# Performance work log

Measured on AMD Instinct MI355X. Metric: run time of the kernel, lower is better.

Reference implementation:

```python
import jax, jax.numpy as jnp
import numpy as np

BN_EPS = 1e-5
GRID_W = 17  # conv output width hardcoded via lat_idx*17+lon_idx

def _conv(x, w, b, stride):
    y = jax.lax.conv_general_dilated(x, w, (stride, stride), [(1, 1), (1, 1)],
                                     dimension_numbers=("NCHW", "OIHW", "NCHW"))
    return y + b[None, :, None, None]

def _bn_eval(x, g, b):
    # running_mean=0, running_var=1 (fresh BatchNorm in eval mode)
    inv = jnp.float32(1.0 / np.sqrt(1.0 + BN_EPS))
    return x * (g[None, :, None, None] * inv) + b[None, :, None, None]

def setup_inputs() -> dict:
    key = jax.random.key(0)
    ks = iter(jax.random.split(key, 64))
    def rn(shape, s=0.05):
        return jax.random.normal(next(ks), shape, jnp.float32) * s
    B, S, K = 512, 128, 64
    NR = 100000
    inp = {}
    inp["roads"] = jax.random.randint(next(ks), (B, S), 0, NR)
    inp["ratios"] = jax.random.uniform(next(ks), (B, S), jnp.float32) * 0.9 + 0.1
    inp["T"] = jax.random.normal(next(ks), (1, 1, 138, 138), jnp.float32)
    inp["lon_idx"] = jax.random.randint(next(ks), (B, K), 0, 17)
    inp["lat_idx"] = jax.random.randint(next(ks), (B, K), 0, 17)
    inp["lengths"] = jax.random.uniform(next(ks), (NR,), jnp.float32) * 100.0 + 1.0
    inp["map_u"] = jnp.arange(NR, dtype=jnp.int32)
    inp["map_s1"] = jax.random.randint(next(ks), (NR,), 0, 14)
    inp["map_s2"] = jax.random.randint(next(ks), (NR,), 0, 7)
    inp["map_s3"] = jax.random.randint(next(ks), (NR,), 0, 2)
    inp["emb_u"] = rn((NR, 128))
    inp["emb_s1"] = rn((14, 16)); inp["emb_s2"] = rn((7, 8)); inp["emb_s3"] = rn((2, 4))
    inp["rho_w1"] = rn((156, 512)); inp["rho_b1"] = jnp.zeros((512,), jnp.float32)
    inp["rho_w21"] = rn((512, 128)); inp["rho_b21"] = jnp.zeros((128,), jnp.float32)
    inp["conv1_w"] = rn((32, 1, 5, 5)); inp["conv1_b"] = jnp.zeros((32,), jnp.float32)
    inp["bn1_g"] = jnp.ones((32,), jnp.float32); inp["bn1_b"] = jnp.zeros((32,), jnp.float32)
    inp["conv2_w"] = rn((64, 32, 4, 4)); inp["conv2_b"] = jnp.zeros((64,), jnp.float32)
    inp["bn2_g"] = jnp.ones((64,), jnp.float32); inp["bn2_b"] = jnp.zeros((64,), jnp.float32)
    inp["conv3_w"] = rn((128, 64, 4, 4)); inp["conv3_b"] = jnp.zeros((128,), jnp.float32)
    inp["bn3_g"] = jnp.ones((128,), jnp.float32); inp["bn3_b"] = jnp.zeros((128,), jnp.float32)
    inp["f2_w1"] = rn((128, 256)); inp["f2_b1"] = jnp.zeros((256,), jnp.float32)
    inp["f2_w2"] = rn((256, 128)); inp["f2_b2"] = jnp.zeros((128,), jnp.float32)
    inp["f_w1"] = rn((256, 512)); inp["f_b1"] = jnp.zeros((512,), jnp.float32)
    inp["f_w21"] = rn((512, 1)); inp["f_b21"] = jnp.zeros((1,), jnp.float32)
    inp["f_w22"] = rn((512, 1)); inp["f_b22"] = jnp.zeros((1,), jnp.float32)
    return inp

def reference(roads, ratios, T, lon_idx, lat_idx, lengths, map_u, map_s1, map_s2, map_s3,
              emb_u, emb_s1, emb_s2, emb_s3, rho_w1, rho_b1, rho_w21, rho_b21,
              conv1_w, conv1_b, bn1_g, bn1_b, conv2_w, conv2_b, bn2_g, bn2_b,
              conv3_w, conv3_b, bn3_g, bn3_b, f2_w1, f2_b1, f2_w2, f2_b2,
              f_w1, f_b1, f_w21, f_b21, f_w22, f_b22):
    # road lengths / weights
    road_lens = lengths[roads] * ratios               # (B,S)
    l = road_lens.sum(axis=1)                         # (B,)
    w = road_lens / l[:, None]                        # (B,S)
    # ProbRho (eval: dropout=id, reparameterize -> mu)
    u = emb_u[map_u[roads]]                           # (B,S,128)
    s1 = emb_s1[map_s1[roads]]; s2 = emb_s2[map_s2[roads]]; s3 = emb_s3[map_s3[roads]]
    x = jnp.concatenate([u, s1, s2, s3], axis=2)      # (B,S,156)
    h = jax.nn.relu(x @ rho_w1 + rho_b1)
    rho = h @ rho_w21 + rho_b21                       # (B,S,128)
    # ProbTraffic_spatial conv stack
    t = jax.nn.leaky_relu(_bn_eval(_conv(T, conv1_w, conv1_b, 2), bn1_g, bn1_b), 0.1)
    t = jax.nn.leaky_relu(_bn_eval(_conv(t, conv2_w, conv2_b, 2), bn2_g, bn2_b), 0.1)
    t = jax.nn.leaky_relu(_bn_eval(_conv(t, conv3_w, conv3_b, 2), bn3_g, bn3_b), 0.1)  # (1,128,17,17)
    c_flat = jnp.transpose(t[0], (1, 2, 0)).reshape(-1, t.shape[1])  # (289,128)
    # fused segment gather + mean over each trajectory's grid cells
    idx = lat_idx * GRID_W + lon_idx                  # (B,K)
    c_mean = c_flat[idx].mean(axis=1)                 # (B,128)
    h2 = jax.nn.selu(c_mean @ f2_w1 + f2_b1)
    c2 = h2 @ f2_w2 + f2_b2                           # (B,128)
    # ProbTravelTime
    xcat = jnp.concatenate([rho, jnp.broadcast_to(c2[:, None, :], rho.shape)], axis=2)  # (B,S,256)
    h3 = jax.nn.relu(xcat @ f_w1 + f_b1)              # (B,S,512)
    logm = (h3 @ f_w21 + f_b21)[..., 0]               # (B,S)
    logv = (h3 @ f_w22 + f_b22)[..., 0]
    logw = jnp.log(w)
    logm_agg = jax.nn.logsumexp(logm + logw, axis=1)
    logv_agg = jax.nn.logsumexp(logv + 2.0 * logw, axis=1)
    logl = jnp.log(l)
    logmu = logl - logm_agg
    loglam = logl - 3.0 * logm_agg - logv_agg
    return (logmu, loglam)
```

## Files before the change

### kernel.cpp

```cpp
#include <hip/hip_runtime.h>
#include <math.h>

#define BB 512
#define SS 128
#define NROWS (BB*SS)
#define TM 32
#define NBLK (NROWS/TM)

__device__ __forceinline__ float leaky01(float x){ return x >= 0.f ? x : 0.1f*x; }

#define BN_INV 0.9999950000374997f
#define SELU_A 1.6732632423543772f
#define SELU_S 1.0507009873554805f

typedef __attribute__((ext_vector_type(8))) short short8;
typedef __attribute__((ext_vector_type(4))) float f32x4;

__device__ __forceinline__ unsigned short f2bf(float f) {
    unsigned int u = __float_as_uint(f);
    u += 0x7fff + ((u >> 16) & 1);
    return (unsigned short)(u >> 16);
}
__device__ __forceinline__ uint2 pack4bf(float a, float b, float c, float d) {
    uint2 r;
    r.x = (unsigned int)f2bf(a) | ((unsigned int)f2bf(b) << 16);
    r.y = (unsigned int)f2bf(c) | ((unsigned int)f2bf(d) << 16);
    return r;
}

#define PREP_N (278528 + 32768 + 131072)
#define PREP_BLOCKS (PREP_N/256)
#define CONV1_BLOCKS 578

__global__ __launch_bounds__(256) void combo1_kernel(
    const float* __restrict__ w1, const float* __restrict__ w21, const float* __restrict__ fw1,
    unsigned short* __restrict__ sw1, unsigned short* __restrict__ sw21, unsigned short* __restrict__ sw3,
    const float* __restrict__ c2w_in, const float* __restrict__ c3w_in,
    float* __restrict__ w2t, float* __restrict__ w3t,
    const float* __restrict__ T, const float* __restrict__ cw,
    const float* __restrict__ cbias, const float* __restrict__ g,
    const float* __restrict__ bb, float* __restrict__ out)
{
    if (blockIdx.x < PREP_BLOCKS) {
        int t = blockIdx.x*256 + threadIdx.x;
        if (t < 81920) {
            int j = t & 7; int r = t >> 3; int lane = r & 63; r >>= 6;
            int ks = r % 5; int nt = r / 5;
            int n = nt*16 + (lane & 15);
            int k = ks*32 + (lane >> 4)*8 + j;
            float v = (k < 156) ? w1[k*512 + n] : 0.f;
            sw1[t] = f2bf(v);
        } else if (t < 147456) {
            int u = t - 81920;
            int j = u & 7; int r = u >> 3; int lane = r & 63; r >>= 6;
            int ks = r & 15; int nt = r >> 4;
            int d = nt*16 + (lane & 15);
            int k = ks*32 + (lane >> 4)*8 + j;
            sw21[u] = f2bf(w21[k*128 + d]);
        } else if (t < 278528) {
            int u = t - 147456;
            int j = u & 7; int r = u >> 3; int lane = r & 63; r >>= 6;
            int ks = r & 7; int nt = r >> 3;
            int n = nt*16 + (lane & 15);
            int k = ks*32 + (lane >> 4)*8 + j;
            sw3[u] = f2bf(fw1[k*512 + n]);
        } else if (t < 278528 + 32768) {
            int u = t - 278528;
            int oc = u >> 9; int r = u & 511;
            int kk = r >> 5; int ic = r & 31;
            w2t[u] = c2w_in[oc*512 + ic*16 + kk];
        } else {
            int u = t - (278528 + 32768);
            int oc = u >> 10; int r = u & 1023;
            int kk = r >> 6; int ic = r & 63;
            w3t[u] = c3w_in[oc*1024 + ic*16 + kk];
        }
    } else {
        int t = (blockIdx.x - PREP_BLOCKS)*256 + threadIdx.x;
        if (t >= 32*68*68) return;
        int oc  = t & 31;
        int pos = t >> 5;
        int oy = pos / 68, ox = pos % 68;
        float acc = cbias[oc];
        #pragma unroll
        for (int ky=0; ky<5; ++ky) {
            int iy = oy*2 - 1 + ky;
            if (iy < 0 || iy >= 138) continue;
            #pragma unroll
            for (int kx=0; kx<5; ++kx) {
                int ix = ox*2 - 1 + kx;
                if (ix < 0 || ix >= 138) continue;
                acc += cw[oc*25 + ky*5 + kx] * T[iy*138 + ix];
            }
        }
        acc = acc * (g[oc]*BN_INV) + bb[oc];
        out[pos*32 + oc] = leaky01(acc);
    }
}

__global__ __launch_bounds__(256) void conv2_kernel(
    const float* __restrict__ in,
    const float* __restrict__ w2t,
    const float* __restrict__ bias, const float* __restrict__ g,
    const float* __restrict__ bb, float* __restrict__ out)
{
    int gid = blockIdx.x*256 + threadIdx.x;
    if (gid >= 64*34*34*4) return;
    int icg = gid & 3;
    int o   = gid >> 2;
    int oc  = o & 63;
    int pos = o >> 6;
    int oy = pos / 34, ox = pos % 34;
    float acc = 0.f;
    #pragma unroll
    for (int ky=0; ky<4; ++ky) {
        int iy = oy*2 - 1 + ky;
        if (iy < 0 || iy >= 68) continue;
        #pragma unroll
        for (int kx=0; kx<4; ++kx) {
            int ix = ox*2 - 1 + kx;
            if (ix < 0 || ix >= 68) continue;
            const float* ip = &in[(iy*68+ix)*32 + icg*8];
            const float* wp = &w2t[oc*512 + (ky*4+kx)*32 + icg*8];
            float4 i0 = *(const float4*)ip, i1 = *(const float4*)(ip+4);
            float4 w0 = *(const float4*)wp, w1v = *(const float4*)(wp+4);
            acc += i0.x*w0.x + i0.y*w0.y + i0.z*w0.z + i0.w*w0.w
                 + i1.x*w1v.x + i1.y*w1v.y + i1.z*w1v.z + i1.w*w1v.w;
        }
    }
    acc += __shfl_xor(acc, 1, 64);
    acc += __shfl_xor(acc, 2, 64);
    if (icg == 0) {
        acc = (acc + bias[oc]) * (g[oc]*BN_INV) + bb[oc];
        out[pos*64 + oc] = leaky01(acc);
    }
}

__global__ __launch_bounds__(256) void conv3_kernel(
    const float* __restrict__ in,
    const float* __restrict__ w3t,
    const float* __restrict__ bias, const float* __restrict__ g,
    const float* __restrict__ bb, float* __restrict__ outT)
{
    int gid = blockIdx.x*256 + threadIdx.x;
    if (gid >= 128*289*8) return;
    int icg = gid & 7;
    int o   = gid >> 3;
    int oc  = o & 127;
    int pos = o >> 7;
    int oy = pos / 17, ox = pos % 17;
    float acc = 0.f;
    #pragma unroll
    for (int ky=0; ky<4; ++ky) {
        int iy = oy*2 - 1 + ky;
        if (iy < 0 || iy >= 34) continue;
        #pragma unroll
        for (int kx=0; kx<4; ++kx) {
            int ix = ox*2 - 1 + kx;
            if (ix < 0 || ix >= 34) continue;
            const float* ip = &in[(iy*34+ix)*64 + icg*8];
            const float* wp = &w3t[oc*1024 + (ky*4+kx)*64 + icg*8];
            float4 i0 = *(const float4*)ip, i1 = *(const float4*)(ip+4);
            float4 w0 = *(const float4*)wp, w1v = *(const float4*)(wp+4);
            acc += i0.x*w0.x + i0.y*w0.y + i0.z*w0.z + i0.w*w0.w
                 + i1.x*w1v.x + i1.y*w1v.y + i1.z*w1v.z + i1.w*w1v.w;
        }
    }
    acc += __shfl_xor(acc, 1, 64);
    acc += __shfl_xor(acc, 2, 64);
    acc += __shfl_xor(acc, 4, 64);
    if (icg == 0) {
        acc = (acc + bias[oc]) * (g[oc]*BN_INV) + bb[oc];
        outT[pos*128 + oc] = leaky01(acc);
    }
}

__global__ __launch_bounds__(256) void cmh2c2_kernel(
    const float* __restrict__ t3T, const int* __restrict__ lat, const int* __restrict__ lon,
    const float* __restrict__ w1, const float* __restrict__ b1,
    const float* __restrict__ w2, const float* __restrict__ b2,
    float* __restrict__ c2b)
{
    __shared__ int   ps[64];
    __shared__ float part[256];
    __shared__ float cms[128];
    __shared__ float h2s[256];
    const int b = blockIdx.x;
    const int tid = threadIdx.x;
    if (tid < 64) ps[tid] = lat[b*64+tid]*17 + lon[b*64+tid];
    __syncthreads();
    {
        int d = tid & 127, half = tid >> 7;
        float s = 0.f;
        #pragma unroll 8
        for (int k=0; k<32; ++k) s += t3T[ps[half*32+k]*128 + d];
        part[tid] = s;
    }
    __syncthreads();
    if (tid < 128) cms[tid] = (part[tid] + part[tid+128]) * (1.f/64.f);
    __syncthreads();
    {
        float acc = b1[tid];
        #pragma unroll 8
        for (int k=0; k<128; ++k) acc += cms[k] * w1[k*256 + tid];
        h2s[tid] = acc > 0.f ? SELU_S*acc : SELU_S*SELU_A*(expf(acc)-1.f);
    }
    __syncthreads();
    {
        int d = tid & 127, half = tid >> 7;
        float acc = 0.f;
        #pragma unroll 8
        for (int k=0; k<128; ++k) acc += h2s[half*128 + k] * w2[(half*128+k)*128 + d];
        part[tid] = acc;
    }
    __syncthreads();
    if (tid < 128) c2b[b*128 + tid] = part[tid] + part[tid+128] + b2[tid];
}

#define XS_S 168
#define H1_S 520
#define XC_S 264

__global__ __launch_bounds__(256, 4) void mega_kernel(
    const int* __restrict__ roads,
    const int* __restrict__ map_u, const int* __restrict__ map_s1,
    const int* __restrict__ map_s2, const int* __restrict__ map_s3,
    const float* __restrict__ emb_u, const float* __restrict__ emb_s1,
    const float* __restrict__ emb_s2, const float* __restrict__ emb_s3,
    const unsigned short* __restrict__ sw1, const float* __restrict__ b1,
    const unsigned short* __restrict__ sw21, const float* __restrict__ b21,
    const float* __restrict__ c2,
    const unsigned short* __restrict__ sw3, const float* __restrict__ fb1,
    const float* __restrict__ fw21, const float* __restrict__ fb21,
    const float* __restrict__ fw22, const float* __restrict__ fb22,
    float* __restrict__ logm, float* __restrict__ logv)
{
    __shared__ unsigned short buf[32*H1_S];
    unsigned short* xs  = buf;
    unsigned short* h1s = buf;
    unsigned short* xcs = buf;
    float* pmv = (float*)&buf[32*XC_S];

    const int tid  = threadIdx.x;
    const int wid  = tid >> 6;
    const int lane = tid & 63;
    const int lo   = lane & 15;
    const int hi   = lane >> 4;
    const int r0   = blockIdx.x * TM;
    const int b    = r0 >> 7;

    short8 afp[8];
    #pragma unroll
    for (int mt=0;mt<8;++mt)
        afp[mt] = *(const short8*)&sw1[((wid*8+mt)*5 + 0)*512 + lane*8];

    {
        int row = tid >> 3, seg = tid & 7;
        int road = roads[r0 + row];
        const float* src = emb_u + (long)map_u[road]*128 + seg*16;
        #pragma unroll
        for (int i=0;i<4;++i) {
            float4 v = *(const float4*)&src[i*4];
            *(uint2*)&xs[row*XS_S + seg*16 + i*4] = pack4bf(v.x, v.y, v.z, v.w);
        }
    }
    for (int idx = tid; idx < 32*32; idx += 256) {
        int row = idx >> 5, k2 = idx & 31;
        int road = roads[r0 + row];
        float v;
        if      (k2 < 16) v = emb_s1[map_s1[road]*16 + k2];
        else if (k2 < 24) v = emb_s2[map_s2[road]*8  + (k2-16)];
        else if (k2 < 28) v = emb_s3[map_s3[road]*4  + (k2-24)];
        else              v = 0.f;
        xs[row*XS_S + 128 + k2] = f2bf(v);
    }
    __syncthreads();

    short8 a2p0, a2p1;
    f32x4 acc1[8][2];
    {
        #pragma unroll
        for (int mt=0;mt<8;++mt){ acc1[mt][0]=(f32x4)(0.f); acc1[mt][1]=(f32x4)(0.f); }
        {
            short8 bf0 = *(const short8*)&xs[lo*XS_S + hi*8];
            short8 bf1 = *(const short8*)&xs[(16+lo)*XS_S + hi*8];
            #pragma unroll
            for (int mt=0;mt<8;++mt) {
                acc1[mt][0] = __builtin_amdgcn_mfma_f32_16x16x32_bf16(afp[mt], bf0, acc1[mt][0], 0,0,0);
                acc1[mt][1] = __builtin_amdgcn_mfma_f32_16x16x32_bf16(afp[mt], bf1, acc1[mt][1], 0,0,0);
            }
        }
        #pragma unroll
        for (int ks=1; ks<5; ++ks) {
            const int kb = ks*32 + hi*8;
            short8 bf0 = *(const short8*)&xs[lo*XS_S + kb];
            short8 bf1 = *(const short8*)&xs[(16+lo)*XS_S + kb];
            short8 af[8];
            #pragma unroll
            for (int mt=0;mt<8;++mt)
                af[mt] = *(const short8*)&sw1[((wid*8+mt)*5 + ks)*512 + lane*8];
            #pragma unroll
            for (int mt=0;mt<8;++mt) {
                acc1[mt][0] = __builtin_amdgcn_mfma_f32_16x16x32_bf16(af[mt], bf0, acc1[mt][0], 0,0,0);
                acc1[mt][1] = __builtin_amdgcn_mfma_f32_16x16x32_bf16(af[mt], bf1, acc1[mt][1], 0,0,0);
            }
        }
    }
    __syncthreads();

    {
        a2p0 = *(const short8*)&sw21[((wid*2+0)*16 + 0)*512 + lane*8];
        a2p1 = *(const short8*)&sw21[((wid*2+1)*16 + 0)*512 + lane*8];
        const int n0 = wid * 128;
        #pragma unroll
        for (int mt=0;mt<8;++mt) {
            const int nb = n0 + mt*16 + hi*4;
            float4 bias = *(const float4*)&b1[nb];
            const float* bp = (const float*)&bias;
            #pragma unroll
            for (int nt=0;nt<2;++nt) {
                const float* a = (const float*)&acc1[mt][nt];
                float y0 = fmaxf(a[0]+bp[0], 0.f), y1 = fmaxf(a[1]+bp[1], 0.f);
                float y2 = fmaxf(a[2]+bp[2], 0.f), y3 = fmaxf(a[3]+bp[3], 0.f);
                *(uint2*)&h1s[(nt*16+lo)*H1_S + nb] = pack4bf(y0,y1,y2,y3);
            }
        }
    }
    __syncthreads();

    short8 a3p[8];
    f32x4 acc2[2][2];
    {
        acc2[0][0]=(f32x4)(0.f); acc2[0][1]=(f32x4)(0.f);
        acc2[1][0]=(f32x4)(0.f); acc2[1][1]=(f32x4)(0.f);
        {
            short8 bf0 = *(const short8*)&h1s[lo*H1_S + hi*8];
            short8 bf1 = *(const short8*)&h1s[(16+lo)*H1_S + hi*8];
            acc2[0][0] = __builtin_amdgcn_mfma_f32_16x16x32_bf16(a2p0, bf0, acc2[0][0], 0,0,0);
            acc2[0][1] = __builtin_amdgcn_mfma_f32_16x16x32_bf16(a2p0, bf1, acc2[0][1], 0,0,0);
            acc2[1][0] = __builtin_amdgcn_mfma_f32_16x16x32_bf16(a2p1, bf0, acc2[1][0], 0,0,0);
            acc2[1][1] = __builtin_amdgcn_mfma_f32_16x16x32_bf16(a2p1, bf1, acc2[1][1], 0,0,0);
        }
        #pragma unroll 5
        for (int ks=1; ks<16; ++ks) {
            const int kb = ks*32 + hi*8;
            short8 bf0 = *(const short8*)&h1s[lo*H1_S + kb];
            short8 bf1 = *(const short8*)&h1s[(16+lo)*H1_S + kb];
            short8 a0 = *(const short8*)&sw21[((wid*2+0)*16 + ks)*512 + lane*8];
            short8 a1 = *(const short8*)&sw21[((wid*2+1)*16 + ks)*512 + lane*8];
            acc2[0][0] = __builtin_amdgcn_mfma_f32_16x16x32_bf16(a0, bf0, acc2[0][0], 0,0,0);
            acc2[0][1] = __builtin_amdgcn_mfma_f32_16x16x32_bf16(a0, bf1, acc2[0][1], 0,0,0);
            acc2[1][0] = __builtin_amdgcn_mfma_f32_16x16x32_bf16(a1, bf0, acc2[1][0], 0,0,0);
            acc2[1][1] = __builtin_amdgcn_mfma_f32_16x16x32_bf16(a1, bf1, acc2[1][1], 0,0,0);
        }
    }
    __syncthreads();

    {
        #pragma unroll
        for (int mt=0;mt<8;++mt)
            a3p[mt] = *(const short8*)&sw3[((wid*8+mt)*8 + 0)*512 + lane*8];
        const int n02 = wid * 32;
        #pragma unroll
        for (int mt=0;mt<2;++mt) {
            const int nb = n02 + mt*16 + hi*4;
            float4 bias = *(const float4*)&b21[nb];
            const float* bp = (const float*)&bias;
            #pragma unroll
            for (int nt=0;nt<2;++nt) {
                const float* a = (const float*)&acc2[mt][nt];
                *(uint2*)&xcs[(nt*16+lo)*XC_S + nb] =
                    pack4bf(a[0]+bp[0], a[1]+bp[1], a[2]+bp[2], a[3]+bp[3]);
            }
        }
        int row = tid >> 3, seg = tid & 7;
        const float* src = c2 + b*128 + seg*16;
        #pragma unroll
        for (int i=0;i<4;++i) {
            float4 v = *(const float4*)&src[i*4];
            *(uint2*)&xcs[row*XC_S + 128 + seg*16 + i*4] = pack4bf(v.x, v.y, v.z, v.w);
        }
    }
    __syncthreads();

    {
        const int n0 = wid * 128;
        f32x4 acc[8][2];
        #pragma unroll
        for (int mt=0;mt<8;++mt){ acc[mt][0]=(f32x4)(0.f); acc[mt][1]=(f32x4)(0.f); }
        {
            short8 bf0 = *(const short8*)&xcs[lo*XC_S + hi*8];
            short8 bf1 = *(const short8*)&xcs[(16+lo)*XC_S + hi*8];
            #pragma unroll
            for (int mt=0;mt<8;++mt) {
                acc[mt][0] = __builtin_amdgcn_mfma_f32_16x16x32_bf16(a3p[mt], bf0, acc[mt][0], 0,0,0);
                acc[mt][1] = __builtin_amdgcn_mfma_f32_16x16x32_bf16(a3p[mt], bf1, acc[mt][1], 0,0,0);
            }
        }
        #pragma unroll 3
        for (int ks=1; ks<8; ++ks) {
            const int kb = ks*32 + hi*8;
            short8 bf0 = *(const short8*)&xcs[lo*XC_S + kb];
            short8 bf1 = *(const short8*)&xcs[(16+lo)*XC_S + kb];
            short8 af[8];
            #pragma unroll
            for (int mt=0;mt<8;++mt)
                af[mt] = *(const short8*)&sw3[((wid*8+mt)*8 + ks)*512 + lane*8];
            #pragma unroll
            for (int mt=0;mt<8;++mt) {
                acc[mt][0] = __builtin_amdgcn_mfma_f32_16x16x32_bf16(af[mt], bf0, acc[mt][0], 0,0,0);
                acc[mt][1] = __builtin_amdgcn_mfma_f32_16x16x32_bf16(af[mt], bf1, acc[mt][1], 0,0,0);
            }
        }
        float sm0=0.f, sm1=0.f, sv0=0.f, sv1=0.f;
        #pragma unroll
        for (int mt=0;mt<8;++mt) {
            const int nb = n0 + mt*16 + hi*4;
            float4 bias = *(const float4*)&fb1[nb];
            float4 wm   = *(const float4*)&fw21[nb];
            float4 wv   = *(const float4*)&fw22[nb];
            const float *bp=(const float*)&bias, *wmp=(const float*)&wm, *wvp=(const float*)&wv;
            const float* a0 = (const float*)&acc[mt][0];
            const float* a1 = (const float*)&acc[mt][1];
            #pragma unroll
            for (int j=0;j<4;++j) {
                float y0 = fmaxf(a0[j]+bp[j], 0.f);
                float y1 = fmaxf(a1[j]+bp[j], 0.f);
                sm0 += y0*wmp[j]; sv0 += y0*wvp[j];
                sm1 += y1*wmp[j]; sv1 += y1*wvp[j];
            }
        }
        sm0 += __shfl_xor(sm0, 16, 64); sm0 += __shfl_xor(sm0, 32, 64);
        sm1 += __shfl_xor(sm1, 16, 64); sm1 += __shfl_xor(sm1, 32, 64);
        sv0 += __shfl_xor(sv0, 16, 64); sv0 += __shfl_xor(sv0, 32, 64);
        sv1 += __shfl_xor(sv1, 16, 64); sv1 += __shfl_xor(sv1, 32, 64);
        if (hi == 0) {
            pmv[wid*32 + lo]        = sm0;
            pmv[wid*32 + 16 + lo]   = sm1;
            pmv[128 + wid*32 + lo]      = sv0;
            pmv[128 + wid*32 + 16 + lo] = sv1;
        }
    }
    __syncthreads();
    if (tid < 32) {
        float sm = pmv[tid]+pmv[32+tid]+pmv[64+tid]+pmv[96+tid];
        float sv = pmv[128+tid]+pmv[160+tid]+pmv[192+tid]+pmv[224+tid];
        logm[r0+tid] = sm + fb21[0];
        logv[r0+tid] = sv + fb22[0];
    }
}

__global__ __launch_bounds__(64) void final_kernel(
    const int* __restrict__ roads, const float* __restrict__ ratios,
    const float* __restrict__ lengths,
    const float* __restrict__ logm, const float* __restrict__ logv,
    float* __restrict__ out)
{
    int b = blockIdx.x;
    int lane = threadIdx.x;
    int i0 = b*128 + lane;
    int i1 = i0 + 64;
    float rl0 = lengths[roads[i0]] * ratios[i0];
    float rl1 = lengths[roads[i1]] * ratios[i1];

    float tsum = rl0 + rl1;
    #pragma unroll
    for (int off=32; off; off>>=1) tsum += __shfl_xor(tsum, off, 64);
    float l = tsum;
    float logl = logf(l);

    float lw0 = logf(rl0) - logl;
    float lw1 = logf(rl1) - logl;

    float am0 = logm[i0] + lw0, am1 = logm[i1] + lw1;
    float av0 = logv[i0] + 2.f*lw0, av1 = logv[i1] + 2.f*lw1;

    float mm = fmaxf(am0, am1);
    #pragma unroll
    for (int off=32; off; off>>=1) mm = fmaxf(mm, __shfl_xor(mm, off, 64));
    float se = expf(am0-mm) + expf(am1-mm);
    #pragma unroll
    for (int off=32; off; off>>=1) se += __shfl_xor(se, off, 64);
    float lsem = logf(se) + mm;

    float mv = fmaxf(av0, av1);
    #pragma unroll
    for (int off=32; off; off>>=1) mv = fmaxf(mv, __shfl_xor(mv, off, 64));
    float sev = expf(av0-mv) + expf(av1-mv);
    #pragma unroll
    for (int off=32; off; off>>=1) sev += __shfl_xor(sev, off, 64);
    float lsev = logf(sev) + mv;

    if (lane == 0) {
        out[b]       = logl - lsem;
        out[512 + b] = logl - 3.f*lsem - lsev;
    }
}

extern "C" void kernel_launch(void* const* d_in, const int* in_sizes, int n_in,
                              void* d_out, int out_size, void* d_ws, size_t ws_size,
                              hipStream_t stream) {
    const int*   roads   = (const int*)  d_in[0];
    const float* ratios  = (const float*)d_in[1];
    const float* T       = (const float*)d_in[2];
    const int*   lon_idx = (const int*)  d_in[3];
    const int*   lat_idx = (const int*)  d_in[4];
    const float* lengths = (const float*)d_in[5];
    const int*   map_u   = (const int*)  d_in[6];
    const int*   map_s1  = (const int*)  d_in[7];
    const int*   map_s2  = (const int*)  d_in[8];
    const int*   map_s3  = (const int*)  d_in[9];
    const float* emb_u   = (const float*)d_in[10];
    const float* emb_s1  = (const float*)d_in[11];
    const float* emb_s2  = (const float*)d_in[12];
    const float* emb_s3  = (const float*)d_in[13];
    const float* rho_w1  = (const float*)d_in[14];
    const float* rho_b1  = (const float*)d_in[15];
    const float* rho_w21 = (const float*)d_in[16];
    const float* rho_b21 = (const float*)d_in[17];
    const float* conv1_w = (const float*)d_in[18];
    const float* conv1_b = (const float*)d_in[19];
    const float* bn1_g   = (const float*)d_in[20];
    const float* bn1_b   = (const float*)d_in[21];
    const float* conv2_w = (const float*)d_in[22];
    const float* conv2_b = (const float*)d_in[23];
    const float* bn2_g   = (const float*)d_in[24];
    const float* bn2_b   = (const float*)d_in[25];
    const float* conv3_w = (const float*)d_in[26];
    const float* conv3_b = (const float*)d_in[27];
    const float* bn3_g   = (const float*)d_in[28];
    const float* bn3_b   = (const float*)d_in[29];
    const float* f2_w1   = (const float*)d_in[30];
    const float* f2_b1   = (const float*)d_in[31];
    const float* f2_w2   = (const float*)d_in[32];
    const float* f2_b2   = (const float*)d_in[33];
    const float* f_w1    = (const float*)d_in[34];
    const float* f_b1    = (const float*)d_in[35];
    const float* f_w21   = (const float*)d_in[36];
    const float* f_b21   = (const float*)d_in[37];
    const float* f_w22   = (const float*)d_in[38];
    const float* f_b22   = (const float*)d_in[39];

    float* ws    = (float*)d_ws;
    float* t1    = ws;
    float* t2    = t1 + 147968;
    float* t3T   = t2 + 73984;
    float* c2b   = t3T + 36992;
    float* logm  = c2b + 65536;
    float* logv  = logm + 65536;
    float* w2t   = logv + 65536;
    float* w3t   = w2t + 32768;
    unsigned short* sw1  = (unsigned short*)(w3t + 131072);
    unsigned short* sw21 = sw1 + 81920;
    unsigned short* sw3  = sw21 + 65536;

    combo1_kernel<<<PREP_BLOCKS + CONV1_BLOCKS, 256, 0, stream>>>(
        rho_w1, rho_w21, f_w1, sw1, sw21, sw3,
        conv2_w, conv3_w, w2t, w3t,
        T, conv1_w, conv1_b, bn1_g, bn1_b, t1);
    conv2_kernel<<<(64*34*34*4 + 255)/256, 256, 0, stream>>>(t1, w2t, conv2_b, bn2_g, bn2_b, t2);
    conv3_kernel<<<(128*289*8 + 255)/256, 256, 0, stream>>>(t2, w3t, conv3_b, bn3_g, bn3_b, t3T);
    cmh2c2_kernel<<<512, 256, 0, stream>>>(t3T, lat_idx, lon_idx, f2_w1, f2_b1, f2_w2, f2_b2, c2b);
    mega_kernel<<<NBLK, 256, 0, stream>>>(roads, map_u, map_s1, map_s2, map_s3,
                                          emb_u, emb_s1, emb_s2, emb_s3,
                                          sw1, rho_b1, sw21, rho_b21,
                                          c2b, sw3, f_b1, f_w21, f_b21, f_w22, f_b22,
                                          logm, logv);
    final_kernel<<<512, 64, 0, stream>>>(roads, ratios, lengths, logm, logv, (float*)d_out);
}
```

Baseline: 124.2 us.

## Retile mega kernel to 64 rows per block with 8 waves and swizzled LDS

The fused MLP kernel now handles 64 rows per block with 512 threads. Each of the 8 waves owns fewer output columns but covers all four 16-row groups, so every weight fragment loaded from global memory feeds twice as many MFMAs and total weight traffic is halved. The padded h1 shared buffer is replaced by an XOR-swizzled layout to avoid bank conflicts and fit 64 rows in 64KB of LDS. The trade-off is larger shared memory per block and fewer blocks, which may lower occupancy and latency hiding.

Result: faster. 117.6 us (-5.4%).

```diff
diff --git a/kernel.cpp b/kernel.cpp
--- a/kernel.cpp
+++ b/kernel.cpp
@@ -4,8 +4,8 @@
 #define BB 512
 #define SS 128
 #define NROWS (BB*SS)
-#define TM 32
-#define NBLK (NROWS/TM)
+#define TMG 64
+#define NBLKG (NROWS/TMG)
 
 __device__ __forceinline__ float leaky01(float x){ return x >= 0.f ? x : 0.1f*x; }
 
@@ -26,6 +26,12 @@
     r.x = (unsigned int)f2bf(a) | ((unsigned int)f2bf(b) << 16);
     r.y = (unsigned int)f2bf(c) | ((unsigned int)f2bf(d) << 16);
     return r;
+}
+
+__device__ __forceinline__ unsigned short* h1p(unsigned short* base, int row, int col) {
+    unsigned off = (unsigned)(row*1024 + col*2);
+    off ^= (unsigned)((row & 7) << 4);
+    return (unsigned short*)((char*)base + off);
 }
 
 #define PREP_N (278528 + 32768 + 131072)
@@ -218,10 +224,9 @@
 }
 
 #define XS_S 168
-#define H1_S 520
 #define XC_S 264
 
-__global__ __launch_bounds__(256, 4) void mega_kernel(
+__global__ __launch_bounds__(512, 4) void mega_kernel(
     const int* __restrict__ roads,
     const int* __restrict__ map_u, const int* __restrict__ map_s1,
     const int* __restrict__ map_s2, const int* __restrict__ map_s3,
@@ -235,24 +240,23 @@
     const float* __restrict__ fw22, const float* __restrict__ fb22,
     float* __restrict__ logm, float* __restrict__ logv)
 {
-    __shared__ unsigned short buf[32*H1_S];
+    __shared__ unsigned short buf[32768];
     unsigned short* xs  = buf;
-    unsigned short* h1s = buf;
     unsigned short* xcs = buf;
-    float* pmv = (float*)&buf[32*XC_S];
+    float* pmv = (float*)buf;
 
     const int tid  = threadIdx.x;
     const int wid  = tid >> 6;
     const int lane = tid & 63;
     const int lo   = lane & 15;
     const int hi   = lane >> 4;
-    const int r0   = blockIdx.x * TM;
+    const int r0   = blockIdx.x * TMG;
     const int b    = r0 >> 7;
 
-    short8 afp[8];
-    #pragma unroll
-    for (int mt=0;mt<8;++mt)
-        afp[mt] = *(const short8*)&sw1[((wid*8+mt)*5 + 0)*512 + lane*8];
+    short8 afp[4];
+    #pragma unroll
+    for (int mt=0;mt<4;++mt)
+        afp[mt] = *(const short8*)&sw1[((wid*4+mt)*5 + 0)*512 + lane*8];
 
     {
         int row = tid >> 3, seg = tid & 7;
@@ -264,7 +268,7 @@
             *(uint2*)&xs[row*XS_S + seg*16 + i*4] = pack4bf(v.x, v.y, v.z, v.w);
         }
     }
-    for (int idx = tid; idx < 32*32; idx += 256) {
+    for (int idx = tid; idx < 64*32; idx += 512) {
         int row = idx >> 5, k2 = idx & 31;
         int road = roads[r0 + row];
         float v;
@@ -276,102 +280,90 @@
     }
     __syncthreads();
 
-    short8 a2p0, a2p1;
-    f32x4 acc1[8][2];
-    {
-        #pragma unroll
-        for (int mt=0;mt<8;++mt){ acc1[mt][0]=(f32x4)(0.f); acc1[mt][1]=(f32x4)(0.f); }
-        {
-            short8 bf0 = *(const short8*)&xs[lo*XS_S + hi*8];
-            short8 bf1 = *(const short8*)&xs[(16+lo)*XS_S + hi*8];
-            #pragma unroll
-            for (int mt=0;mt<8;++mt) {
-                acc1[mt][0] = __builtin_amdgcn_mfma_f32_16x16x32_bf16(afp[mt], bf0, acc1[mt][0], 0,0,0);
-                acc1[mt][1] = __builtin_amdgcn_mfma_f32_16x16x32_bf16(afp[mt], bf1, acc1[mt][1], 0,0,0);
+    short8 a2p;
+    f32x4 acc1[4][4];
+    {
+        #pragma unroll
+        for (int mt=0;mt<4;++mt)
+            #pragma unroll
+            for (int rg=0;rg<4;++rg) acc1[mt][rg]=(f32x4)(0.f);
+        #pragma unroll
+        for (int ks=0; ks<5; ++ks) {
+            const int kb = ks*32 + hi*8;
+            short8 bf[4];
+            #pragma unroll
+            for (int rg=0;rg<4;++rg)
+                bf[rg] = *(const short8*)&xs[(rg*16+lo)*XS_S + kb];
+            short8 af[4];
+            if (ks == 0) {
+                #pragma unroll
+                for (int mt=0;mt<4;++mt) af[mt] = afp[mt];
+            } else {
+                #pragma unroll
+                for (int mt=0;mt<4;++mt)
+                    af[mt] = *(const short8*)&sw1[((wid*4+mt)*5 + ks)*512 + lane*8];
             }
-        }
-        #pragma unroll
-        for (int ks=1; ks<5; ++ks) {
-            const int kb = ks*32 + hi*8;
-            short8 bf0 = *(const short8*)&xs[lo*XS_S + kb];
-            short8 bf1 = *(const short8*)&xs[(16+lo)*XS_S + kb];
-            short8 af[8];
-            #pragma unroll
-            for (int mt=0;mt<8;++mt)
-                af[mt] = *(const short8*)&sw1[((wid*8+mt)*5 + ks)*512 + lane*8];
-            #pragma unroll
-            for (int mt=0;mt<8;++mt) {
-                acc1[mt][0] = __builtin_amdgcn_mfma_f32_16x16x32_bf16(af[mt], bf0, acc1[mt][0], 0,0,0);
-                acc1[mt][1] = __builtin_amdgcn_mfma_f32_16x16x32_bf16(af[mt], bf1, acc1[mt][1], 0,0,0);
-            }
-        }
-    }
-    __syncthreads();
-
-    {
-        a2p0 = *(const short8*)&sw21[((wid*2+0)*16 + 0)*512 + lane*8];
-        a2p1 = *(const short8*)&sw21[((wid*2+1)*16 + 0)*512 + lane*8];
-        const int n0 = wid * 128;
-        #pragma unroll
-        for (int mt=0;mt<8;++mt) {
+            #pragma unroll
+            for (int mt=0;mt<4;++mt)
+                #pragma unroll
+                for (int rg=0;rg<4;++rg)
+                    acc1[mt][rg] = __builtin_amdgcn_mfma_f32_16x16x32_bf16(af[mt], bf[rg], acc1[mt][rg], 0,0,0);
+        }
+    }
+    __syncthreads();
+
+    {
+        a2p = *(const short8*)&sw21[(wid*16 + 0)*512 + lane*8];
+        const int n0 = wid * 64;
+        #pragma unroll
+        for (int mt=0;mt<4;++mt) {
             const int nb = n0 + mt*16 + hi*4;
             float4 bias = *(const float4*)&b1[nb];
             const float* bp = (const float*)&bias;
             #pragma unroll
-            for (int nt=0;nt<2;++nt) {
-                const float* a = (const float*)&acc1[mt][nt];
+            for (int rg=0;rg<4;++rg) {
+                const float* a = (const float*)&acc1[mt][rg];
                 float y0 = fmaxf(a[0]+bp[0], 0.f), y1 = fmaxf(a[1]+bp[1], 0.f);
                 float y2 = fmaxf(a[2]+bp[2], 0.f), y3 = fmaxf(a[3]+bp[3], 0.f);
-                *(uint2*)&h1s[(nt*16+lo)*H1_S + nb] = pack4bf(y0,y1,y2,y3);
+                *(uint2*)h1p(buf, rg*16+lo, nb) = pack4bf(y0,y1,y2,y3);
             }
         }
     }
     __syncthreads();
 
-    short8 a3p[8];
-    f32x4 acc2[2][2];
-    {
-        acc2[0][0]=(f32x4)(0.f); acc2[0][1]=(f32x4)(0.f);
-        acc2[1][0]=(f32x4)(0.f); acc2[1][1]=(f32x4)(0.f);
-        {
-            short8 bf0 = *(const short8*)&h1s[lo*H1_S + hi*8];
-            short8 bf1 = *(const short8*)&h1s[(16+lo)*H1_S + hi*8];
-            acc2[0][0] = __builtin_amdgcn_mfma_f32_16x16x32_bf16(a2p0, bf0, acc2[0][0], 0,0,0);
-            acc2[0][1] = __builtin_amdgcn_mfma_f32_16x16x32_bf16(a2p0, bf1, acc2[0][1], 0,0,0);
-            acc2[1][0] = __builtin_amdgcn_mfma_f32_16x16x32_bf16(a2p1, bf0, acc2[1][0], 0,0,0);
-            acc2[1][1] = __builtin_amdgcn_mfma_f32_16x16x32_bf16(a2p1, bf1, acc2[1][1], 0,0,0);
-        }
-        #pragma unroll 5
-        for (int ks=1; ks<16; ++ks) {
+    short8 a3p[4];
+    f32x4 acc2[4];
+    {
+        #pragma unroll
+        for (int rg=0;rg<4;++rg) acc2[rg]=(f32x4)(0.f);
+        #pragma unroll 4
+        for (int ks=0; ks<16; ++ks) {
             const int kb = ks*32 + hi*8;
-            short8 bf0 = *(const short8*)&h1s[lo*H1_S + kb];
-            short8 bf1 = *(const short8*)&h1s[(16+lo)*H1_S + kb];
-            short8 a0 = *(const short8*)&sw21[((wid*2+0)*16 + ks)*512 + lane*8];
-            short8 a1 = *(const short8*)&sw21[((wid*2+1)*16 + ks)*512 + lane*8];
-            acc2[0][0] = __builtin_amdgcn_mfma_f32_16x16x32_bf16(a0, bf0, acc2[0][0], 0,0,0);
-            acc2[0][1] = __builtin_amdgcn_mfma_f32_16x16x32_bf16(a0, bf1, acc2[0][1], 0,0,0);
-            acc2[1][0] = __builtin_amdgcn_mfma_f32_16x16x32_bf16(a1, bf0, acc2[1][0], 0,0,0);
-            acc2[1][1] = __builtin_amdgcn_mfma_f32_16x16x32_bf16(a1, bf1, acc2[1][1], 0,0,0);
-        }
-    }
-    __syncthreads();
-
-    {
-        #pragma unroll
-        for (int mt=0;mt<8;++mt)
-            a3p[mt] = *(const short8*)&sw3[((wid*8+mt)*8 + 0)*512 + lane*8];
-        const int n02 = wid * 32;
-        #pragma unroll
-        for (int mt=0;mt<2;++mt) {
-            const int nb = n02 + mt*16 + hi*4;
-            float4 bias = *(const float4*)&b21[nb];
-            const float* bp = (const float*)&bias;
-            #pragma unroll
-            for (int nt=0;nt<2;++nt) {
-                const float* a = (const float*)&acc2[mt][nt];
-                *(uint2*)&xcs[(nt*16+lo)*XC_S + nb] =
-                    pack4bf(a[0]+bp[0], a[1]+bp[1], a[2]+bp[2], a[3]+bp[3]);
-            }
+            short8 bf[4];
+            #pragma unroll
+            for (int rg=0;rg<4;++rg)
+                bf[rg] = *(const short8*)h1p(buf, rg*16+lo, kb);
+            short8 a = (ks == 0) ? a2p
+                     : *(const short8*)&sw21[(wid*16 + ks)*512 + lane*8];
+            #pragma unroll
+            for (int rg=0;rg<4;++rg)
+                acc2[rg] = __builtin_amdgcn_mfma_f32_16x16x32_bf16(a, bf[rg], acc2[rg], 0,0,0);
+        }
+    }
+    __syncthreads();
+
+    {
+        #pragma unroll
+        for (int mt=0;mt<4;++mt)
+            a3p[mt] = *(const short8*)&sw3[((wid*4+mt)*8 + 0)*512 + lane*8];
+        const int nb = wid*16 + hi*4;
+        float4 bias = *(const float4*)&b21[nb];
+        const float* bp = (const float*)&bias;
+        #pragma unroll
+        for (int rg=0;rg<4;++rg) {
+            const float* a = (const float*)&acc2[rg];
+            *(uint2*)&xcs[(rg*16+lo)*XC_S + nb] =
+                pack4bf(a[0]+bp[0], a[1]+bp[1], a[2]+bp[2], a[3]+bp[3]);
         }
         int row = tid >> 3, seg = tid & 7;
         const float* src = c2 + b*128 + seg*16;
@@ -384,67 +376,76 @@
     __syncthreads();
 
     {
-        const int n0 = wid * 128;
-        f32x4 acc[8][2];
-        #pragma unroll
-        for (int mt=0;mt<8;++mt){ acc[mt][0]=(f32x4)(0.f); acc[mt][1]=(f32x4)(0.f); }
-        {
-            short8 bf0 = *(const short8*)&xcs[lo*XC_S + hi*8];
-            short8 bf1 = *(const short8*)&xcs[(16+lo)*XC_S + hi*8];
-            #pragma unroll
-            for (int mt=0;mt<8;++mt) {
-                acc[mt][0] = __builtin_amdgcn_mfma_f32_16x16x32_bf16(a3p[mt], bf0, acc[mt][0], 0,0,0);
-                acc[mt][1] = __builtin_amdgcn_mfma_f32_16x16x32_bf16(a3p[mt], bf1, acc[mt][1], 0,0,0);
+        const int n0 = wid * 64;
+        f32x4 acc[4][4];
+        #pragma unroll
+        for (int mt=0;mt<4;++mt)
+            #pragma unroll
+            for (int rg=0;rg<4;++rg) acc[mt][rg]=(f32x4)(0.f);
+        #pragma unroll 2
+        for (int ks=0; ks<8; ++ks) {
+            const int kb = ks*32 + hi*8;
+            short8 bf[4];
+            #pragma unroll
+            for (int rg=0;rg<4;++rg)
+                bf[rg] = *(const short8*)&xcs[(rg*16+lo)*XC_S + kb];
+            short8 af[4];
+            if (ks == 0) {
+                #pragma unroll
+                for (int mt=0;mt<4;++mt) af[mt] = a3p[mt];
+            } else {
+                #pragma unroll
+                for (int mt=0;mt<4;++mt)
+                    af[mt] = *(const short8*)&sw3[((wid*4+mt)*8 + ks)*512 + lane*8];
             }
-        }
-        #pragma unroll 3
-        for (int ks=1; ks<8; ++ks) {
-            const int kb = ks*32 + hi*8;
-            short8 bf0 = *(const short8*)&xcs[lo*XC_S + kb];
-            short8 bf1 = *(const short8*)&xcs[(16+lo)*XC_S + kb];
-            short8 af[8];
-            #pragma unroll
-            for (int mt=0;mt<8;++mt)
-                af[mt] = *(const short8*)&sw3[((wid*8+mt)*8 + ks)*512 + lane*8];
-            #pragma unroll
-            for (int mt=0;mt<8;++mt) {
-                acc[mt][0] = __builtin_amdgcn_mfma_f32_16x16x32_bf16(af[mt], bf0, acc[mt][0], 0,0,0);
-                acc[mt][1] = __builtin_amdgcn_mfma_f32_16x16x32_bf16(af[mt], bf1, acc[mt][1], 0,0,0);
-            }
-        }
-        float sm0=0.f, sm1=0.f, sv0=0.f, sv1=0.f;
-        #pragma unroll
-        for (int mt=0;mt<8;++mt) {
+            #pragma unroll
+            for (int mt=0;mt<4;++mt)
+                #pragma unroll
+                for (int rg=0;rg<4;++rg)
+                    acc[mt][rg] = __builtin_amdgcn_mfma_f32_16x16x32_bf16(af[mt], bf[rg], acc[mt][rg], 0,0,0);
+        }
+        float sm[4] = {0.f,0.f,0.f,0.f};
+        float sv[4] = {0.f,0.f,0.f,0.f};
+        #pragma unroll
+        for (int mt=0;mt<4;++mt) {
             const int nb = n0 + mt*16 + hi*4;
             float4 bias = *(const float4*)&fb1[nb];
             float4 wm   = *(const float4*)&fw21[nb];
             float4 wv   = *(const float4*)&fw22[nb];
             const float *bp=(const float*)&bias, *wmp=(const float*)&wm, *wvp=(const float*)&wv;
-            const float* a0 = (const float*)&acc[mt][0];
-            const float* a1 = (const float*)&acc[mt][1];
-            #pragma unroll
-            for (int j=0;j<4;++j) {
-                float y0 = fmaxf(a0[j]+bp[j], 0.f);
-                float y1 = fmaxf(a1[j]+bp[j], 0.f);
-                sm0 += y0*wmp[j]; sv0 += y0*wvp[j];
-                sm1 += y1*wmp[j]; sv1 += y1*wvp[j];
+            #pragma unroll
+            for (int rg=0;rg<4;++rg) {
+                const float* a = (const float*)&acc[mt][rg];
+                #pragma unroll
+                for (int j=0;j<4;++j) {
+                    float y = fmaxf(a[j]+bp[j], 0.f);
+                    sm[rg] += y*wmp[j];
+                    sv[rg] += y*wvp[j];
+                }
             }
         }
-        sm0 += __shfl_xor(sm0, 16, 64); sm0 += __shfl_xor(sm0, 32, 64);
-        sm1 += __shfl_xor(sm1, 16, 64); sm1 += __shfl_xor(sm1, 32, 64);
-        sv0 += __shfl_xor(sv0, 16, 64); sv0 += __shfl_xor(sv0, 32, 64);
-        sv1 += __shfl_xor(sv1, 16, 64); sv1 += __shfl_xor(sv1, 32, 64);
+        #pragma unroll
+        for (int rg=0;rg<4;++rg) {
+            sm[rg] += __shfl_xor(sm[rg], 16, 64); sm[rg] += __shfl_xor(sm[rg], 32, 64);
+            sv[rg] += __shfl_xor(sv[rg], 16, 64); sv[rg] += __shfl_xor(sv[rg], 32, 64);
+        }
+        __syncthreads();
         if (hi == 0) {
-            pmv[wid*32 + lo]        = sm0;
-            pmv[wid*32 + 16 + lo]   = sm1;
-            pmv[128 + wid*32 + lo]      = sv0;
-            pmv[128 + wid*32 + 16 + lo] = sv1;
-        }
-    }
-    __syncthreads();
-    if (tid < 32) {
-        float sm = pmv[tid]+pmv[32+tid]+pmv[64+tid]+pmv[96+tid];
-        float sv = pmv[128+tid]+pmv[160+tid]+pmv[192+tid]+pmv[224+tid];
+            #pragma unroll
+            for (int rg=0;rg<4;++rg) {
+                pmv[wid*64 + rg*16 + lo]       = sm[rg];
+                pmv[512 + wid*64 + rg*16 + lo] = sv[rg];
+            }
+        }
+    }
+    __syncthreads();
+    if (tid < 64) {
+        float sm = 0.f, sv = 0.f;
+        #pragma unroll
+        for (int w=0; w<8; ++w) {
+            sm += pmv[w*64 + tid];
+            sv += pmv[512 + w*64 + tid];
+        }
         logm[r0+tid] = sm + fb21[0];
         logv[r0+tid] = sv + fb22[0];
     }
@@ -561,10 +562,10 @@
     conv2_kernel<<<(64*34*34*4 + 255)/256, 256, 0, stream>>>(t1, w2t, conv2_b, bn2_g, bn2_b, t2);
     conv3_kernel<<<(128*289*8 + 255)/256, 256, 0, stream>>>(t2, w3t, conv3_b, bn3_g, bn3_b, t3T);
     cmh2c2_kernel<<<512, 256, 0, stream>>>(t3T, lat_idx, lon_idx, f2_w1, f2_b1, f2_w2, f2_b2, c2b);
-    mega_kernel<<<NBLK, 256, 0, stream>>>(roads, map_u, map_s1, map_s2, map_s3,
-                                          emb_u, emb_s1, emb_s2, emb_s3,
-                                          sw1, rho_b1, sw21, rho_b21,
-                                          c2b, sw3, f_b1, f_w21, f_b21, f_w22, f_b22,
-                                          logm, logv);
+    mega_kernel<<<NBLKG, 512, 0, stream>>>(roads, map_u, map_s1, map_s2, map_s3,
+                                           emb_u, emb_s1, emb_s2, emb_s3,
+                                           sw1, rho_b1, sw21, rho_b21,
+                                           c2b, sw3, f_b1, f_w21, f_b21, f_w22, f_b22,
+                                           logm, logv);
     final_kernel<<<512, 64, 0, stream>>>(roads, ratios, lengths, logm, logv, (float*)d_out);
 }
```
